# Kernel optimization log

Hardware: AMD Instinct MI355X
Metric: run time of the kernel (lower is better)

Reference implementation:

```python
import jax, jax.numpy as jnp
import numpy as np

B, S, D, E, H = 8, 1024, 1024, 8, 4096  # batch, seq, n_embd, num_experts, 4*n_embd


def setup_inputs() -> dict:
    key = jax.random.key(0)
    ks = jax.random.split(key, 8)
    sc = 0.02
    return {
        "x": jax.random.normal(ks[0], (B, S, D), jnp.float32),
        "noise": jax.random.normal(ks[1], (B, S, E), jnp.float32),
        "Wg": jax.random.normal(ks[2], (D, E), jnp.float32) * sc,
        "bg": jnp.zeros((E,), jnp.float32),
        "Wn": jax.random.normal(ks[3], (D, E), jnp.float32) * sc,
        "bn": jnp.zeros((E,), jnp.float32),
        "W1": jax.random.normal(ks[4], (E, D, H), jnp.float32) * sc,
        "b1": jnp.zeros((E, H), jnp.float32),
        "W2": jax.random.normal(ks[5], (E, H, D), jnp.float32) * sc,
        "b2": jnp.zeros((E, D), jnp.float32),
        "top_k": 2,
    }


def reference(x, noise, Wg, bg, Wn, bn, W1, b1, W2, b2, top_k):
    # --- NoisyTopkRouter ---
    logits = jnp.einsum("bsd,de->bse", x, Wg) + bg
    noise_logits = jnp.einsum("bsd,de->bse", x, Wn) + bn
    noisy = logits + noise * jax.nn.softplus(noise_logits)  # [B,S,E]
    _, idx = jax.lax.top_k(noisy, top_k)  # [B,S,K]
    in_topk = jax.nn.one_hot(idx, noisy.shape[-1], dtype=noisy.dtype).sum(-2) > 0
    sparse_logits = jnp.where(in_topk, noisy, -jnp.inf)
    gating = jax.nn.softmax(sparse_logits, axis=-1)  # zero outside top-k

    # --- dispatch/combine: gating is exactly zero for non-selected experts,
    # so per-expert masked gather + weighted scatter-add == gated dense sum ---
    g_e = jnp.moveaxis(gating, -1, 0)  # [E,B,S]

    def body(acc, params):
        W1e, b1e, W2e, b2e, ge = params
        h = jax.nn.relu(jnp.einsum("bsd,dh->bsh", x, W1e) + b1e)  # [B,S,H]
        y = (jnp.einsum("bsh,hd->bsd", h, W2e) + b2e) * ge[..., None]
        return acc + y, y

    final_output, expert_outputs = jax.lax.scan(
        body, jnp.zeros_like(x), (W1, b1, W2, b2, g_e)
    )
    # expert_outputs: [E,B,S,D], matching the per-expert weighted outputs list
    return final_output, expert_outputs, gating
```

## Files before the change

### kernel.cpp

```cpp
#include <hip/hip_runtime.h>
#include <hip/hip_bf16.h>
#include <stdint.h>

#define TKN   8192
#define DD    1024
#define EE    8
#define HH    4096
#define TOPK  2
#define NASG  (TKN * TOPK)
#define NSLOT 72

typedef unsigned short u16;
typedef __bf16 bf16x8 __attribute__((ext_vector_type(8)));
typedef float  f32x4  __attribute__((ext_vector_type(4)));

__device__ __forceinline__ u16 f2bf(float f) {
  __hip_bfloat16 h = __float2bfloat16(f);
  return __builtin_bit_cast(u16, h);
}
__device__ __forceinline__ float bf2f(u16 u) {
  uint32_t v = ((uint32_t)u) << 16;
  return __builtin_bit_cast(float, v);
}

__device__ __forceinline__ void glds16(const void* g, void* l) {
  __builtin_amdgcn_global_load_lds(
      (__attribute__((address_space(1))) void*)g,
      (__attribute__((address_space(3))) void*)l, 16, 0, 0);
}

#define FENCE() asm volatile("" ::: "memory")
#define BAR()   do { FENCE(); __builtin_amdgcn_s_barrier(); FENCE(); } while (0)
#define VMCNT0() asm volatile("s_waitcnt vmcnt(0)" ::: "memory")

__global__ __launch_bounds__(256) void transpose_cvt_kernel(
    const float* __restrict__ src, u16* __restrict__ dst, int R, int C) {
  __shared__ float tile[64][33];
  int e = blockIdx.z;
  int c0 = blockIdx.x * 32, r0 = blockIdx.y * 64;
  int tx = threadIdx.x, ty = threadIdx.y;
  const float* s = src + (size_t)e * R * C;
  uint32_t* d32 = (uint32_t*)(dst + (size_t)e * R * C);
#pragma unroll
  for (int j = 0; j < 8; j++)
    tile[ty * 8 + j][tx] = s[(size_t)(r0 + ty * 8 + j) * C + c0 + tx];
  __syncthreads();
#pragma unroll
  for (int jj = 0; jj < 4; jj++) {
    int c = c0 + ty * 4 + jj;
    uint32_t lo = f2bf(tile[2 * tx][ty * 4 + jj]);
    uint32_t hi = f2bf(tile[2 * tx + 1][ty * 4 + jj]);
    d32[((size_t)c * R + r0) / 2 + tx] = lo | (hi << 16);
  }
}

__global__ __launch_bounds__(256) void router_kernel(
    const float* __restrict__ x, const float* __restrict__ noise,
    const float* __restrict__ Wg, const float* __restrict__ bg,
    const float* __restrict__ Wn, const float* __restrict__ bn,
    float* __restrict__ gating, u16* __restrict__ xb,
    int* __restrict__ sel_e, float* __restrict__ sel_g) {
  int t = blockIdx.x;
  int tid = threadIdx.x;
  float acc[16];
#pragma unroll
  for (int j = 0; j < 16; j++) acc[j] = 0.f;
  for (int i = tid; i < DD; i += 256) {
    float xv = x[(size_t)t * DD + i];
    xb[(size_t)t * DD + i] = f2bf(xv);
    const float4* g4 = (const float4*)(Wg + (size_t)i * EE);
    const float4* n4 = (const float4*)(Wn + (size_t)i * EE);
    float4 ga = g4[0], gb = g4[1];
    float4 na = n4[0], nb = n4[1];
    acc[0] += xv * ga.x;  acc[1] += xv * ga.y;  acc[2] += xv * ga.z;  acc[3] += xv * ga.w;
    acc[4] += xv * gb.x;  acc[5] += xv * gb.y;  acc[6] += xv * gb.z;  acc[7] += xv * gb.w;
    acc[8] += xv * na.x;  acc[9] += xv * na.y;  acc[10] += xv * na.z; acc[11] += xv * na.w;
    acc[12] += xv * nb.x; acc[13] += xv * nb.y; acc[14] += xv * nb.z; acc[15] += xv * nb.w;
  }
  __shared__ float red[4][16];
  int lane = tid & 63, wv = tid >> 6;
#pragma unroll
  for (int j = 0; j < 16; j++) {
    float v = acc[j];
    for (int o = 32; o > 0; o >>= 1) v += __shfl_down(v, o);
    acc[j] = v;
  }
  if (lane == 0) {
#pragma unroll
    for (int j = 0; j < 16; j++) red[wv][j] = acc[j];
  }
  __syncthreads();
  if (tid == 0) {
    float nz[EE];
#pragma unroll
    for (int e = 0; e < EE; e++) {
      float dg = red[0][e] + red[1][e] + red[2][e] + red[3][e] + bg[e];
      float dn = red[0][8 + e] + red[1][8 + e] + red[2][8 + e] + red[3][8 + e] + bn[e];
      float sp = fmaxf(dn, 0.f) + log1pf(expf(-fabsf(dn)));
      nz[e] = dg + noise[(size_t)t * EE + e] * sp;
    }
    int m1 = 0;
    for (int e = 1; e < EE; e++) if (nz[e] > nz[m1]) m1 = e;
    int m2 = (m1 == 0) ? 1 : 0;
    for (int e = 0; e < EE; e++) if (e != m1 && nz[e] > nz[m2]) m2 = e;
    float eb = expf(nz[m2] - nz[m1]);
    float den = 1.f + eb;
    float g1 = 1.f / den, g2 = eb / den;
    gating[(size_t)t * EE + m1] = g1;
    gating[(size_t)t * EE + m2] = g2;
    sel_e[t * 2] = m1; sel_e[t * 2 + 1] = m2;
    sel_g[t * 2] = g1; sel_g[t * 2 + 1] = g2;
  }
}

__global__ __launch_bounds__(256) void hist_scan_kernel(
    const int* __restrict__ sel_e, int* __restrict__ counts,
    int* __restrict__ offsets, int* __restrict__ cursors,
    int* __restrict__ slots) {
  __shared__ int hist[EE];
  int tid = threadIdx.x;
  if (tid < EE) hist[tid] = 0;
  __syncthreads();
  for (int i = tid; i < NASG; i += 256) atomicAdd(&hist[sel_e[i]], 1);
  __syncthreads();
  if (tid == 0) {
    int off = 0, ns = 0;
    for (int e = 0; e < EE; e++) {
      int c = hist[e];
      counts[e] = c; offsets[e] = off; cursors[e] = off; off += c;
      int nrt = (c + 255) >> 8;
      for (int rt = 0; rt < nrt; rt++) slots[ns++] = (e << 16) | rt;
    }
    for (; ns < NSLOT; ns++) slots[ns] = -1;
  }
}

__global__ __launch_bounds__(256) void build_lists_kernel(
    const int* __restrict__ sel_e, const float* __restrict__ sel_g,
    int* __restrict__ cursors, int* __restrict__ tok_list,
    float* __restrict__ gate_list, int* __restrict__ asg_of) {
  int t = blockIdx.x * 256 + threadIdx.x;
  int lane = threadIdx.x & 63;
#pragma unroll
  for (int k = 0; k < TOPK; k++) {
    int e = sel_e[t * 2 + k];
    float g = sel_g[t * 2 + k];
    for (int ee = 0; ee < EE; ee++) {
      unsigned long long m = __ballot(e == ee);
      if (m) {
        int leader = __ffsll(m) - 1;
        int base = 0;
        if (lane == leader) base = atomicAdd(&cursors[ee], __popcll(m));
        base = __shfl(base, leader);
        if (e == ee) {
          int slot = base + __popcll(m & ((1ull << lane) - 1ull));
          tok_list[slot] = t;
          gate_list[slot] = g;
          asg_of[t * 2 + k] = slot;
        }
      }
    }
  }
}

__global__ __launch_bounds__(256) void zerofill_kernel(
    const float* __restrict__ gating, float* __restrict__ expert_out) {
  int id = blockIdx.x;
  int e = id >> 13, t = id & (TKN - 1);
  if (gating[(size_t)t * EE + e] != 0.f) return;
  float4* p = (float4*)(expert_out + ((size_t)e * TKN + t) * DD);
  p[threadIdx.x] = (float4){0.f, 0.f, 0.f, 0.f};
}

__global__ __launch_bounds__(256) void combine_kernel(
    const float* __restrict__ expert_out, const int* __restrict__ sel_e,
    float* __restrict__ final_out) {
  int t = blockIdx.x;
  int e1 = sel_e[2 * t], e2 = sel_e[2 * t + 1];
  const float4* r1 = (const float4*)(expert_out + ((size_t)e1 * TKN + t) * DD);
  const float4* r2 = (const float4*)(expert_out + ((size_t)e2 * TKN + t) * DD);
  float4* o = (float4*)(final_out + (size_t)t * DD);
  int i = threadIdx.x;
  float4 a = r1[i], b = r2[i];
  o[i] = (float4){a.x + b.x, a.y + b.y, a.z + b.z, a.w + b.w};
}

__global__ __launch_bounds__(256) void merge_combine_kernel(
    const u16* __restrict__ part, const int* __restrict__ asg_of,
    const int* __restrict__ sel_e, const float* __restrict__ sel_g,
    const float* __restrict__ b2, float* __restrict__ expert_out,
    float* __restrict__ final_out) {
  int t = blockIdx.x;
  int i = threadIdx.x;
  int i1 = asg_of[2 * t], i2 = asg_of[2 * t + 1];
  int e1 = sel_e[2 * t], e2 = sel_e[2 * t + 1];
  float g1 = sel_g[2 * t], g2 = sel_g[2 * t + 1];
  float s1[4] = {0.f, 0.f, 0.f, 0.f}, s2[4] = {0.f, 0.f, 0.f, 0.f};
#pragma unroll
  for (int kq = 0; kq < 4; kq++) {
    ushort4 a = ((const ushort4*)(part + ((size_t)kq * NASG + i1) * DD))[i];
    ushort4 b = ((const ushort4*)(part + ((size_t)kq * NASG + i2) * DD))[i];
    s1[0] += bf2f(a.x); s1[1] += bf2f(a.y); s1[2] += bf2f(a.z); s1[3] += bf2f(a.w);
    s2[0] += bf2f(b.x); s2[1] += bf2f(b.y); s2[2] += bf2f(b.z); s2[3] += bf2f(b.w);
  }
  float4 bb1 = ((const float4*)(b2 + (size_t)e1 * DD))[i];
  float4 bb2 = ((const float4*)(b2 + (size_t)e2 * DD))[i];
  float4 y1 = {(s1[0] + bb1.x) * g1, (s1[1] + bb1.y) * g1,
               (s1[2] + bb1.z) * g1, (s1[3] + bb1.w) * g1};
  float4 y2 = {(s2[0] + bb2.x) * g2, (s2[1] + bb2.y) * g2,
               (s2[2] + bb2.z) * g2, (s2[3] + bb2.w) * g2};
  ((float4*)(expert_out + ((size_t)e1 * TKN + t) * DD))[i] = y1;
  ((float4*)(expert_out + ((size_t)e2 * TKN + t) * DD))[i] = y2;
  ((float4*)(final_out + (size_t)t * DD))[i] =
      (float4){y1.x + y2.x, y1.y + y2.y, y1.z + y2.z, y1.w + y2.w};
}

template<int KLOOP, int KSTRIDE, bool GATHER, int EPI, int LOGC>
__global__ __launch_bounds__(512, 2) void gemm8_kernel(
    const u16* __restrict__ A, const u16* __restrict__ Bm,
    const float* __restrict__ bias, const int* __restrict__ tok_list,
    const float* __restrict__ gate_list, const int* __restrict__ counts,
    const int* __restrict__ offsets, const int* __restrict__ slots,
    int Ncols, u16* __restrict__ OutBf, float* __restrict__ outF,
    u16* __restrict__ outP) {
  constexpr int NT = KLOOP / 64;
  int gid = blockIdx.x;
  int q = gid >> 3;
  constexpr int PERX = 9 << LOGC;
  int kq = q / PERX;
  int r0q = q - kq * PERX;
  int slot = (gid & 7) * 9 + (r0q >> LOGC);
  int ct = r0q & ((1 << LOGC) - 1);
  int packed = slots[slot];
  if (packed < 0) return;
  int e = packed >> 16;
  int rt = packed & 0xffff;
  int cnt = counts[e];
  int off = offsets[e];
  int col0 = ct * 256;
  int k0e = kq * KLOOP;

  __shared__ __attribute__((aligned(16))) char ldsc[131072];

  int tid = threadIdx.x;
  int w = tid >> 6, l = tid & 63;
  int wm = w >> 2, wn = w & 3;
  int fr = l & 15, hi = l >> 4;
  int kk16 = hi << 4;
  int xr = (fr & 7) << 4;

  int rl0 = w * 8 + (l >> 3);
  int slotE = ((l & 7) ^ ((l >> 3) & 7)) << 3;
  const u16* aptr[4];
  const u16* bptr[4];
#pragma unroll
  for (int i = 0; i < 4; i++) {
    int r = rt * 256 + rl0 + i * 64;
    if (GATHER) {
      int idx = min(off + r, NASG - 1);
      aptr[i] = A + (size_t)tok_list[idx] * KSTRIDE + k0e + slotE;
    } else {
      aptr[i] = A + (size_t)(off + r) * KSTRIDE + k0e + slotE;
    }
    bptr[i] = Bm + ((size_t)e * Ncols + col0 + rl0 + i * 64) * KSTRIDE + k0e + slotE;
  }
  char* ldsA = ldsc;
  char* ldsB = ldsc + 65536;

  auto issueAB = [&](int t) {
    char* db = ldsB + (t & 1) * 32768 + w * 1024;
    char* da = ldsA + (t & 1) * 32768 + w * 1024;
    glds16(bptr[0] + t * 64, db);
    glds16(bptr[1] + t * 64, db + 8192);
    glds16(bptr[2] + t * 64, db + 16384);
    glds16(bptr[3] + t * 64, db + 24576);
    glds16(aptr[0] + t * 64, da);
    glds16(aptr[1] + t * 64, da + 8192);
    glds16(aptr[2] + t * 64, da + 16384);
    glds16(aptr[3] + t * 64, da + 24576);
  };

  f32x4 acc[8][4];
#pragma unroll
  for (int m = 0; m < 8; m++)
#pragma unroll
    for (int n = 0; n < 4; n++) acc[m][n] = (f32x4){0.f, 0.f, 0.f, 0.f};
  bf16x8 aF[4][2], bF0[2][2], bF1[2][2];

  issueAB(0);
  VMCNT0();
  BAR();

  for (int t = 0; t < NT; t++) {
    int abase = (t & 1) * 32768;
    int bbase = 65536 + (t & 1) * 32768;
    if (t + 1 < NT) issueAB(t + 1);
#pragma unroll
    for (int mm = 0; mm < 4; mm++)
#pragma unroll
      for (int ks = 0; ks < 2; ks++)
        aF[mm][ks] = *(const bf16x8*)(ldsc + abase + (wm * 128 + mm * 16 + fr) * 128 +
                                      ((ks * 64 + kk16) ^ xr));
#pragma unroll
    for (int nn = 0; nn < 2; nn++)
#pragma unroll
      for (int ks = 0; ks < 2; ks++) {
        bF0[nn][ks] = *(const bf16x8*)(ldsc + bbase + (wn * 64 + nn * 16 + fr) * 128 +
                                       ((ks * 64 + kk16) ^ xr));
        bF1[nn][ks] = *(const bf16x8*)(ldsc + bbase + (wn * 64 + 32 + nn * 16 + fr) * 128 +
                                       ((ks * 64 + kk16) ^ xr));
      }
    __builtin_amdgcn_s_setprio(1);
#pragma unroll
    for (int mm = 0; mm < 4; mm++)
#pragma unroll
      for (int nn = 0; nn < 2; nn++)
#pragma unroll
        for (int ks = 0; ks < 2; ks++) {
          acc[mm][nn]     = __builtin_amdgcn_mfma_f32_16x16x32_bf16(aF[mm][ks], bF0[nn][ks], acc[mm][nn], 0, 0, 0);
          acc[mm][2 + nn] = __builtin_amdgcn_mfma_f32_16x16x32_bf16(aF[mm][ks], bF1[nn][ks], acc[mm][2 + nn], 0, 0, 0);
        }
    __builtin_amdgcn_s_setprio(0);
#pragma unroll
    for (int mm = 0; mm < 4; mm++)
#pragma unroll
      for (int ks = 0; ks < 2; ks++)
        aF[mm][ks] = *(const bf16x8*)(ldsc + abase + (wm * 128 + 64 + mm * 16 + fr) * 128 +
                                      ((ks * 64 + kk16) ^ xr));
    __builtin_amdgcn_s_setprio(1);
#pragma unroll
    for (int mm = 0; mm < 4; mm++)
#pragma unroll
      for (int nn = 0; nn < 2; nn++)
#pragma unroll
        for (int ks = 0; ks < 2; ks++) {
          acc[4 + mm][nn]     = __builtin_amdgcn_mfma_f32_16x16x32_bf16(aF[mm][ks], bF0[nn][ks], acc[4 + mm][nn], 0, 0, 0);
          acc[4 + mm][2 + nn] = __builtin_amdgcn_mfma_f32_16x16x32_bf16(aF[mm][ks], bF1[nn][ks], acc[4 + mm][2 + nn], 0, 0, 0);
        }
    __builtin_amdgcn_s_setprio(0);
    VMCNT0();
    BAR();
  }

  float biasN[4];
  int cN[4];
#pragma unroll
  for (int n = 0; n < 4; n++) {
    cN[n] = col0 + wn * 64 + (n >> 1) * 32 + (n & 1) * 16 + fr;
    biasN[n] = (EPI == 2) ? 0.f : bias[e * Ncols + cN[n]];
  }
  if constexpr (EPI == 0) {
#pragma unroll
    for (int m = 0; m < 8; m++) {
      int rb = rt * 256 + wm * 128 + (m >> 2) * 64 + (m & 3) * 16 + hi * 4;
#pragma unroll
      for (int j = 0; j < 4; j++) {
        int r = rb + j;
        if (r < cnt) {
#pragma unroll
          for (int n = 0; n < 4; n++) {
            float v = acc[m][n][j] + biasN[n];
            OutBf[(size_t)(off + r) * Ncols + cN[n]] = f2bf(fmaxf(v, 0.f));
          }
        }
      }
    }
  } else if constexpr (EPI == 1) {
#pragma unroll
    for (int m = 0; m < 8; m++) {
      int rb = rt * 256 + wm * 128 + (m >> 2) * 64 + (m & 3) * 16 + hi * 4;
#pragma unroll
      for (int j = 0; j < 4; j++) {
        int r = rb + j;
        if (r < cnt) {
          int idx = off + r;
          int tok = tok_list[idx];
          float g = gate_list[idx];
          size_t erow = ((size_t)e * TKN + tok) * DD;
#pragma unroll
          for (int n = 0; n < 4; n++)
            outF[erow + cN[n]] = (acc[m][n][j] + biasN[n]) * g;
        }
      }
    }
  } else {
#pragma unroll
    for (int m = 0; m < 8; m++) {
      int rb = rt * 256 + wm * 128 + (m >> 2) * 64 + (m & 3) * 16 + hi * 4;
#pragma unroll
      for (int j = 0; j < 4; j++) {
        int r = rb + j;
        if (r < cnt) {
          size_t prow = ((size_t)kq * NASG + off + r) * DD;
#pragma unroll
          for (int n = 0; n < 4; n++)
            outP[prow + cN[n]] = f2bf(acc[m][n][j]);
        }
      }
    }
  }
}

extern "C" void kernel_launch(void* const* d_in, const int* in_sizes, int n_in,
                              void* d_out, int out_size, void* d_ws, size_t ws_size,
                              hipStream_t stream) {
  const float* x     = (const float*)d_in[0];
  const float* noise = (const float*)d_in[1];
  const float* Wg    = (const float*)d_in[2];
  const float* bg    = (const float*)d_in[3];
  const float* Wn    = (const float*)d_in[4];
  const float* bn    = (const float*)d_in[5];
  const float* W1    = (const float*)d_in[6];
  const float* b1    = (const float*)d_in[7];
  const float* W2    = (const float*)d_in[8];
  const float* b2    = (const float*)d_in[9];

  float* final_out  = (float*)d_out;
  float* expert_out = final_out + (size_t)TKN * DD;
  float* gating     = expert_out + (size_t)EE * TKN * DD;

  char* ws = (char*)d_ws;
  size_t o = 0;
  auto alloc = [&](size_t bytes) {
    char* p = ws + o;
    o += bytes;
    o = (o + 255) & ~(size_t)255;
    return p;
  };
  u16*   xb        = (u16*)alloc((size_t)TKN * DD * 2);
  u16*   w1t       = (u16*)alloc((size_t)EE * HH * DD * 2);
  u16*   w2t       = (u16*)alloc((size_t)EE * DD * HH * 2);
  u16*   hbuf      = (u16*)alloc(((size_t)NASG + 256) * HH * 2);
  int*   tok_list  = (int*)alloc((size_t)NASG * 4);
  float* gate_list = (float*)alloc((size_t)NASG * 4);
  int*   sel_e     = (int*)alloc((size_t)NASG * 4);
  float* sel_g     = (float*)alloc((size_t)NASG * 4);
  int*   asg_of    = (int*)alloc((size_t)NASG * 4);
  int*   counts    = (int*)alloc(256);
  int*   offsets   = (int*)alloc(256);
  int*   cursors   = (int*)alloc(256);
  int*   slots     = (int*)alloc(NSLOT * 4);
  u16*   part      = (u16*)alloc((size_t)4 * NASG * DD * 2);
  bool use_split = (o <= ws_size);

  hipMemsetAsync(gating, 0, (size_t)TKN * EE * sizeof(float), stream);

  router_kernel<<<TKN, 256, 0, stream>>>(x, noise, Wg, bg, Wn, bn, gating, xb, sel_e, sel_g);
  hist_scan_kernel<<<1, 256, 0, stream>>>(sel_e, counts, offsets, cursors, slots);
  build_lists_kernel<<<TKN / 256, 256, 0, stream>>>(sel_e, sel_g, cursors, tok_list,
                                                    gate_list, asg_of);
  zerofill_kernel<<<EE * TKN, 256, 0, stream>>>(gating, expert_out);

  transpose_cvt_kernel<<<dim3(HH / 32, DD / 64, EE), dim3(32, 8), 0, stream>>>(W1, w1t, DD, HH);
  transpose_cvt_kernel<<<dim3(DD / 32, HH / 64, EE), dim3(32, 8), 0, stream>>>(W2, w2t, HH, DD);

  gemm8_kernel<DD, DD, true, 0, 4><<<8 * 9 * 16, 512, 0, stream>>>(
      xb, w1t, b1, tok_list, nullptr, counts, offsets, slots, HH, hbuf, nullptr, nullptr);

  if (use_split) {
    gemm8_kernel<HH / 4, HH, false, 2, 2><<<8 * 9 * 4 * 4, 512, 0, stream>>>(
        hbuf, w2t, b2, tok_list, gate_list, counts, offsets, slots, DD, nullptr, nullptr, part);
    merge_combine_kernel<<<TKN, 256, 0, stream>>>(part, asg_of, sel_e, sel_g, b2,
                                                  expert_out, final_out);
  } else {
    gemm8_kernel<HH, HH, false, 1, 2><<<8 * 9 * 4, 512, 0, stream>>>(
        hbuf, w2t, b2, tok_list, gate_list, counts, offsets, slots, DD, nullptr, expert_out, nullptr);
    combine_kernel<<<TKN, 256, 0, stream>>>(expert_out, sel_e, final_out);
  }
}
```

Measured before the change: 611.1 us.

## Fuse zero-fill into router and finalize kernels; stagger MFMA phases across warp rows

The router now writes every gating entry, so the memset goes away. The finalize kernel writes zeros for the non-selected expert rows, so the separate zerofill pass over expert_out runs only on the non-split path. The GEMM main loop is split by warp row: wm!=0 warps delay their high-half MFMAs into the next iteration, so the two warp groups interleave LDS reads and MFMA work. This saves a launch and a read-check pass over gating and expert_out, but the staggered schedule adds code size and register-pressure risk.

```diff
diff --git a/kernel.cpp b/kernel.cpp
--- a/kernel.cpp
+++ b/kernel.cpp
@@ -106,8 +106,9 @@
     float eb = expf(nz[m2] - nz[m1]);
     float den = 1.f + eb;
     float g1 = 1.f / den, g2 = eb / den;
-    gating[(size_t)t * EE + m1] = g1;
-    gating[(size_t)t * EE + m2] = g2;
+#pragma unroll
+    for (int e = 0; e < EE; e++)
+      gating[(size_t)t * EE + e] = (e == m1) ? g1 : (e == m2) ? g2 : 0.f;
     sel_e[t * 2] = m1; sel_e[t * 2 + 1] = m2;
     sel_g[t * 2] = g1; sel_g[t * 2 + 1] = g2;
   }
@@ -185,7 +186,7 @@
   o[i] = (float4){a.x + b.x, a.y + b.y, a.z + b.z, a.w + b.w};
 }
 
-__global__ __launch_bounds__(256) void merge_combine_kernel(
+__global__ __launch_bounds__(256) void finalize_kernel(
     const u16* __restrict__ part, const int* __restrict__ asg_of,
     const int* __restrict__ sel_e, const float* __restrict__ sel_g,
     const float* __restrict__ b2, float* __restrict__ expert_out,
@@ -209,8 +210,12 @@
                (s1[2] + bb1.z) * g1, (s1[3] + bb1.w) * g1};
   float4 y2 = {(s2[0] + bb2.x) * g2, (s2[1] + bb2.y) * g2,
                (s2[2] + bb2.z) * g2, (s2[3] + bb2.w) * g2};
-  ((float4*)(expert_out + ((size_t)e1 * TKN + t) * DD))[i] = y1;
-  ((float4*)(expert_out + ((size_t)e2 * TKN + t) * DD))[i] = y2;
+  float4 z = {0.f, 0.f, 0.f, 0.f};
+#pragma unroll
+  for (int e = 0; e < EE; e++) {
+    float4 v = (e == e1) ? y1 : (e == e2) ? y2 : z;
+    ((float4*)(expert_out + ((size_t)e * TKN + t) * DD))[i] = v;
+  }
   ((float4*)(final_out + (size_t)t * DD))[i] =
       (float4){y1.x + y2.x, y1.y + y2.y, y1.z + y2.z, y1.w + y2.w};
 }
@@ -287,29 +292,32 @@
     for (int n = 0; n < 4; n++) acc[m][n] = (f32x4){0.f, 0.f, 0.f, 0.f};
   bf16x8 aF[4][2], bF0[2][2], bF1[2][2];
 
-  issueAB(0);
-  VMCNT0();
-  BAR();
-
-  for (int t = 0; t < NT; t++) {
-    int abase = (t & 1) * 32768;
-    int bbase = 65536 + (t & 1) * 32768;
-    if (t + 1 < NT) issueAB(t + 1);
+  auto RLOB = [&](int ab, int bb) {
 #pragma unroll
     for (int mm = 0; mm < 4; mm++)
 #pragma unroll
       for (int ks = 0; ks < 2; ks++)
-        aF[mm][ks] = *(const bf16x8*)(ldsc + abase + (wm * 128 + mm * 16 + fr) * 128 +
+        aF[mm][ks] = *(const bf16x8*)(ldsc + ab + (wm * 128 + mm * 16 + fr) * 128 +
                                       ((ks * 64 + kk16) ^ xr));
 #pragma unroll
     for (int nn = 0; nn < 2; nn++)
 #pragma unroll
       for (int ks = 0; ks < 2; ks++) {
-        bF0[nn][ks] = *(const bf16x8*)(ldsc + bbase + (wn * 64 + nn * 16 + fr) * 128 +
+        bF0[nn][ks] = *(const bf16x8*)(ldsc + bb + (wn * 64 + nn * 16 + fr) * 128 +
                                        ((ks * 64 + kk16) ^ xr));
-        bF1[nn][ks] = *(const bf16x8*)(ldsc + bbase + (wn * 64 + 32 + nn * 16 + fr) * 128 +
+        bF1[nn][ks] = *(const bf16x8*)(ldsc + bb + (wn * 64 + 32 + nn * 16 + fr) * 128 +
                                        ((ks * 64 + kk16) ^ xr));
       }
+  };
+  auto RHI = [&](int ab) {
+#pragma unroll
+    for (int mm = 0; mm < 4; mm++)
+#pragma unroll
+      for (int ks = 0; ks < 2; ks++)
+        aF[mm][ks] = *(const bf16x8*)(ldsc + ab + (wm * 128 + 64 + mm * 16 + fr) * 128 +
+                                      ((ks * 64 + kk16) ^ xr));
+  };
+  auto MLO = [&]() {
     __builtin_amdgcn_s_setprio(1);
 #pragma unroll
     for (int mm = 0; mm < 4; mm++)
@@ -321,12 +329,8 @@
           acc[mm][2 + nn] = __builtin_amdgcn_mfma_f32_16x16x32_bf16(aF[mm][ks], bF1[nn][ks], acc[mm][2 + nn], 0, 0, 0);
         }
     __builtin_amdgcn_s_setprio(0);
-#pragma unroll
-    for (int mm = 0; mm < 4; mm++)
-#pragma unroll
-      for (int ks = 0; ks < 2; ks++)
-        aF[mm][ks] = *(const bf16x8*)(ldsc + abase + (wm * 128 + 64 + mm * 16 + fr) * 128 +
-                                      ((ks * 64 + kk16) ^ xr));
+  };
+  auto MHI = [&]() {
     __builtin_amdgcn_s_setprio(1);
 #pragma unroll
     for (int mm = 0; mm < 4; mm++)
@@ -338,8 +342,37 @@
           acc[4 + mm][2 + nn] = __builtin_amdgcn_mfma_f32_16x16x32_bf16(aF[mm][ks], bF1[nn][ks], acc[4 + mm][2 + nn], 0, 0, 0);
         }
     __builtin_amdgcn_s_setprio(0);
-    VMCNT0();
-    BAR();
+  };
+
+  issueAB(0);
+  VMCNT0();
+  BAR();
+
+  if (wm == 0) {
+    for (int t = 0; t < NT; t++) {
+      int ab = (t & 1) * 32768;
+      int bb = 65536 + (t & 1) * 32768;
+      if (t + 1 < NT) issueAB(t + 1);
+      RLOB(ab, bb);
+      MLO();
+      RHI(ab);
+      MHI();
+      VMCNT0();
+      BAR();
+    }
+  } else {
+    for (int t = 0; t < NT; t++) {
+      int ab = (t & 1) * 32768;
+      int bb = 65536 + (t & 1) * 32768;
+      if (t + 1 < NT) issueAB(t + 1);
+      if (t > 0) MHI();
+      RLOB(ab, bb);
+      MLO();
+      RHI(ab);
+      VMCNT0();
+      BAR();
+    }
+    MHI();
   }
 
   float biasN[4];
@@ -443,13 +476,10 @@
   u16*   part      = (u16*)alloc((size_t)4 * NASG * DD * 2);
   bool use_split = (o <= ws_size);
 
-  hipMemsetAsync(gating, 0, (size_t)TKN * EE * sizeof(float), stream);
-
   router_kernel<<<TKN, 256, 0, stream>>>(x, noise, Wg, bg, Wn, bn, gating, xb, sel_e, sel_g);
   hist_scan_kernel<<<1, 256, 0, stream>>>(sel_e, counts, offsets, cursors, slots);
   build_lists_kernel<<<TKN / 256, 256, 0, stream>>>(sel_e, sel_g, cursors, tok_list,
                                                     gate_list, asg_of);
-  zerofill_kernel<<<EE * TKN, 256, 0, stream>>>(gating, expert_out);
 
   transpose_cvt_kernel<<<dim3(HH / 32, DD / 64, EE), dim3(32, 8), 0, stream>>>(W1, w1t, DD, HH);
   transpose_cvt_kernel<<<dim3(DD / 32, HH / 64, EE), dim3(32, 8), 0, stream>>>(W2, w2t, HH, DD);
@@ -460,9 +490,10 @@
   if (use_split) {
     gemm8_kernel<HH / 4, HH, false, 2, 2><<<8 * 9 * 4 * 4, 512, 0, stream>>>(
         hbuf, w2t, b2, tok_list, gate_list, counts, offsets, slots, DD, nullptr, nullptr, part);
-    merge_combine_kernel<<<TKN, 256, 0, stream>>>(part, asg_of, sel_e, sel_g, b2,
-                                                  expert_out, final_out);
+    finalize_kernel<<<TKN, 256, 0, stream>>>(part, asg_of, sel_e, sel_g, b2,
+                                             expert_out, final_out);
   } else {
+    zerofill_kernel<<<EE * TKN, 256, 0, stream>>>(gating, expert_out);
     gemm8_kernel<HH, HH, false, 1, 2><<<8 * 9 * 4, 512, 0, stream>>>(
         hbuf, w2t, b2, tok_list, gate_list, counts, offsets, slots, DD, nullptr, expert_out, nullptr);
     combine_kernel<<<TKN, 256, 0, stream>>>(expert_out, sel_e, final_out);
```

Result: no change. 606.0 us (-0.8%).
